# Optimization experiments

Measured on AMD Instinct MI355X. Metric: run time of the kernel, lower is better.

The kernel has to match this reference:

```python
import jax, jax.numpy as jnp
import numpy as np


def setup_inputs() -> dict:
    key = jax.random.key(0)
    k1, k2 = jax.random.split(key)
    N, C, H, W = 4, 32, 512, 512
    src = jax.random.normal(k1, (N, C, H, W), dtype=jnp.float32)
    # flow: per-pixel displacement in pixels, channels [dx, dy]
    flow = jax.random.normal(k2, (N, 2, H, W), dtype=jnp.float32) * 3.0
    return {"src": src, "flow": flow}


def reference(src, flow):
    """SpatialTransformer.forward(src, flow, train=True): identity grid + flow,
    normalize to [-1,1], then manual bilinear_grid_sample (align_corners=True)."""
    N, C, H, W = src.shape
    dt = flow.dtype

    # identity grid: stack(meshgrid(arange(H), arange(W)))[[1,0]] -> (x, y) channels
    yy, xx = jnp.meshgrid(jnp.arange(H, dtype=dt), jnp.arange(W, dtype=dt), indexing='ij')
    grid = jnp.stack([xx, yy])[None]          # (1, 2, H, W)
    new_locs = grid + flow                    # (N, 2, H, W)

    # normalize: shape = [W, H]; channel 0 (x) by W-1, channel 1 (y) by H-1
    xn = 2.0 * (new_locs[:, 0] / (W - 1) - 0.5)   # (N, H, W)
    yn = 2.0 * (new_locs[:, 1] / (H - 1) - 0.5)

    # bilinear_grid_sample, align_corners=True: unnormalize back to pixel coords
    x = (xn + 1.0) / 2.0 * (W - 1)
    y = (yn + 1.0) / 2.0 * (H - 1)

    x0 = jnp.floor(x)
    y0 = jnp.floor(y)
    x1 = x0 + 1.0
    y1 = y0 + 1.0

    wa = (x1 - x) * (y1 - y)   # weight for (x0, y0)
    wb = (x1 - x) * (y - y0)   # weight for (x0, y1)
    wc = (x - x0) * (y1 - y)   # weight for (x1, y0)
    wd = (x - x0) * (y - y0)   # weight for (x1, y1)

    # zero-pad image by 1 pixel on each side, shift indices by +1, clamp
    im_p = jnp.pad(src, ((0, 0), (0, 0), (1, 1), (1, 1)))  # (N, C, H+2, W+2)
    Hp, Wp = H + 2, W + 2
    xi0 = jnp.clip(x0.astype(jnp.int32) + 1, 0, Wp - 1)
    xi1 = jnp.clip(x1.astype(jnp.int32) + 1, 0, Wp - 1)
    yi0 = jnp.clip(y0.astype(jnp.int32) + 1, 0, Hp - 1)
    yi1 = jnp.clip(y1.astype(jnp.int32) + 1, 0, Hp - 1)

    def gather(im, yi, xi):  # im: (C, Hp, Wp); yi, xi: (H, W) -> (C, H, W)
        return im[:, yi, xi]

    Ia = jax.vmap(gather)(im_p, yi0, xi0)
    Ib = jax.vmap(gather)(im_p, yi1, xi0)
    Ic = jax.vmap(gather)(im_p, yi0, xi1)
    Id = jax.vmap(gather)(im_p, yi1, xi1)

    out = (Ia * wa[:, None] + Ib * wb[:, None]
           + Ic * wc[:, None] + Id * wd[:, None])   # (N, C, H, W)
    return out
```

## Files before the change

### kernel.cpp

```cpp
#include <hip/hip_runtime.h>
#include <hip/hip_bf16.h>


constexpr int N_ = 4, C_ = 32, H_ = 512, W_ = 512;
constexpr size_t PLANE = (size_t)H_ * W_;

__global__ __launch_bounds__(256) void nchw_to_nhwc(
    const float* __restrict__ in, float* __restrict__ out) {
    __shared__ float lds[256][33];

    int b = blockIdx.x;
    int n = b >> 10;
    int pb = (b & 1023) << 8;

    int t = threadIdx.x;

    {
        int c = t >> 3;
        int j = t & 7;
        const float* ip = in + ((size_t)n * C_ + c) * PLANE + pb;
        #pragma unroll
        for (int it = 0; it < 8; ++it) {
            int p_off = it * 32 + j * 4;
            float4 v = *(const float4*)(ip + p_off);
            lds[p_off + 0][c] = v.x;
            lds[p_off + 1][c] = v.y;
            lds[p_off + 2][c] = v.z;
            lds[p_off + 3][c] = v.w;
        }
    }
    __syncthreads();

    {
        int q = t & 7;
        int u = t >> 3;
        float* op = out + ((size_t)n * PLANE + pb) * C_;
        #pragma unroll
        for (int it = 0; it < 8; ++it) {
            int p_local = it * 32 + u;
            float4 v;
            v.x = lds[p_local][q * 4 + 0];
            v.y = lds[p_local][q * 4 + 1];
            v.z = lds[p_local][q * 4 + 2];
            v.w = lds[p_local][q * 4 + 3];
            *(float4*)(op + (size_t)p_local * C_ + q * 4) = v;
        }
    }
}

__global__ __launch_bounds__(256) void st_warp_nhwc(
    const float* __restrict__ srcT, const float* __restrict__ flow,
    float* __restrict__ out) {
    int t = blockIdx.x * blockDim.x + threadIdx.x;
    int q = t & 7;
    int g = t >> 3;

    int w = g & (W_ - 1);
    int h = (g >> 9) & (H_ - 1);
    int n = g >> 18;

    const float* f = flow + (size_t)n * 2 * PLANE + (size_t)h * W_ + w;
    float fx = f[0];
    float fy = f[PLANE];

    float xl = (float)w + fx;
    float yl = (float)h + fy;
    float xn = 2.0f * (xl / (float)(W_ - 1) - 0.5f);
    float yn = 2.0f * (yl / (float)(H_ - 1) - 0.5f);
    float x = (xn + 1.0f) / 2.0f * (float)(W_ - 1);
    float y = (yn + 1.0f) / 2.0f * (float)(H_ - 1);

    float x0f = floorf(x), y0f = floorf(y);
    float x1f = x0f + 1.0f, y1f = y0f + 1.0f;

    int ix0 = (int)x0f, iy0 = (int)y0f;

    int xa = min(max(ix0 + 1, 0), W_ + 1) - 1;
    int xb = min(max(ix0 + 2, 0), W_ + 1) - 1;
    int ya = min(max(iy0 + 1, 0), H_ + 1) - 1;
    int yb = min(max(iy0 + 2, 0), H_ + 1) - 1;

    float vxa = ((unsigned)xa < (unsigned)W_) ? 1.0f : 0.0f;
    float vxb = ((unsigned)xb < (unsigned)W_) ? 1.0f : 0.0f;
    float vya = ((unsigned)ya < (unsigned)H_) ? 1.0f : 0.0f;
    float vyb = ((unsigned)yb < (unsigned)H_) ? 1.0f : 0.0f;

    float ax = (x1f - x) * vxa;
    float bx = (x - x0f) * vxb;
    float ay = (y1f - y) * vya;
    float by = (y - y0f) * vyb;

    float wa = ax * ay;
    float wb = ax * by;
    float wc = bx * ay;
    float wd = bx * by;

    int xac = min(max(xa, 0), W_ - 1);
    int xbc = min(max(xb, 0), W_ - 1);
    int yac = min(max(ya, 0), H_ - 1);
    int ybc = min(max(yb, 0), H_ - 1);

    const float* sp = srcT + (size_t)n * PLANE * C_ + (size_t)q * 4;
    const float4 A = *(const float4*)(sp + (size_t)(yac * W_ + xac) * C_);
    const float4 B = *(const float4*)(sp + (size_t)(ybc * W_ + xac) * C_);
    const float4 Cv = *(const float4*)(sp + (size_t)(yac * W_ + xbc) * C_);
    const float4 D = *(const float4*)(sp + (size_t)(ybc * W_ + xbc) * C_);

    float r0 = A.x * wa + B.x * wb + Cv.x * wc + D.x * wd;
    float r1 = A.y * wa + B.y * wb + Cv.y * wc + D.y * wd;
    float r2 = A.z * wa + B.z * wb + Cv.z * wc + D.z * wd;
    float r3 = A.w * wa + B.w * wb + Cv.w * wc + D.w * wd;

    float* op = out + ((size_t)n * C_ + 4 * q) * PLANE + (size_t)h * W_ + w;
    op[0] = r0;
    op[PLANE] = r1;
    op[2 * PLANE] = r2;
    op[3 * PLANE] = r3;
}

__global__ __launch_bounds__(256) void st_warp_direct(
    const float* __restrict__ src, const float* __restrict__ flow,
    float* __restrict__ out) {
    int idx = blockIdx.x * blockDim.x + threadIdx.x;
    if (idx >= N_ * H_ * W_) return;
    int w = idx & (W_ - 1);
    int h = (idx >> 9) & (H_ - 1);
    int n = idx >> 18;
    const float* f = flow + (size_t)n * 2 * PLANE + (size_t)h * W_ + w;
    float fx = f[0], fy = f[PLANE];
    float xl = (float)w + fx, yl = (float)h + fy;
    float xn = 2.0f * (xl / (float)(W_ - 1) - 0.5f);
    float yn = 2.0f * (yl / (float)(H_ - 1) - 0.5f);
    float x = (xn + 1.0f) / 2.0f * (float)(W_ - 1);
    float y = (yn + 1.0f) / 2.0f * (float)(H_ - 1);
    float x0f = floorf(x), y0f = floorf(y);
    float x1f = x0f + 1.0f, y1f = y0f + 1.0f;
    int ix0 = (int)x0f, iy0 = (int)y0f;
    int xa = min(max(ix0 + 1, 0), W_ + 1) - 1;
    int xb = min(max(ix0 + 2, 0), W_ + 1) - 1;
    int ya = min(max(iy0 + 1, 0), H_ + 1) - 1;
    int yb = min(max(iy0 + 2, 0), H_ + 1) - 1;
    float vxa = ((unsigned)xa < (unsigned)W_) ? 1.0f : 0.0f;
    float vxb = ((unsigned)xb < (unsigned)W_) ? 1.0f : 0.0f;
    float vya = ((unsigned)ya < (unsigned)H_) ? 1.0f : 0.0f;
    float vyb = ((unsigned)yb < (unsigned)H_) ? 1.0f : 0.0f;
    float ax = (x1f - x) * vxa, bx = (x - x0f) * vxb;
    float ay = (y1f - y) * vya, by = (y - y0f) * vyb;
    float wa = ax * ay, wb = ax * by, wc = bx * ay, wd = bx * by;
    int xac = min(max(xa, 0), W_ - 1), xbc = min(max(xb, 0), W_ - 1);
    int yac = min(max(ya, 0), H_ - 1), ybc = min(max(yb, 0), H_ - 1);
    int o00 = yac * W_ + xac, o01 = ybc * W_ + xac;
    int o10 = yac * W_ + xbc, o11 = ybc * W_ + xbc;
    const float* sp = src + (size_t)n * C_ * PLANE;
    float* op = out + (size_t)n * C_ * PLANE + (size_t)h * W_ + w;
    #pragma unroll 4
    for (int c = 0; c < C_; ++c) {
        const float* s = sp + (size_t)c * PLANE;
        float v = s[o00] * wa + s[o01] * wb + s[o10] * wc + s[o11] * wd;
        op[(size_t)c * PLANE] = v;
    }
}

extern "C" void kernel_launch(void* const* d_in, const int* in_sizes, int n_in,
                              void* d_out, int out_size, void* d_ws, size_t ws_size,
                              hipStream_t stream) {
    const float* src  = (const float*)d_in[0];
    const float* flow = (const float*)d_in[1];
    float* out = (float*)d_out;

    const size_t need = (size_t)N_ * C_ * PLANE * sizeof(float);
    if (ws_size >= need) {
        float* srcT = (float*)d_ws;
        nchw_to_nhwc<<<4096, 256, 0, stream>>>(src, srcT);
        int total = N_ * H_ * W_ * 8;
        st_warp_nhwc<<<total / 256, 256, 0, stream>>>(srcT, flow, out);
    } else {
        int total = N_ * H_ * W_;
        st_warp_direct<<<(total + 255) / 256, 256, 0, stream>>>(src, flow, out);
    }
}
```

Measured before the change: 318.3 us.

## Process two rows per thread with swizzled block order and nontemporal stores

The warp kernel now has each thread handle two vertically adjacent output pixels for its channel quad, which halves the grid to 16384 blocks and loads flow for both rows up front. Block IDs are swizzled so that consecutively scheduled blocks land in different chunks of the image, likely to spread work across XCDs or channels while keeping gather locality. Output writes use nontemporal stores so streamed results do not pollute caches needed for the source gathers. The risks are less parallelism and more register pressure per thread, and the swizzle could hurt L2 locality if neighbouring blocks end up on different dies.

```diff
diff --git a/kernel.cpp b/kernel.cpp
--- a/kernel.cpp
+++ b/kernel.cpp
@@ -48,74 +48,89 @@
     }
 }
 
-__global__ __launch_bounds__(256) void st_warp_nhwc(
+__global__ __launch_bounds__(256) void st_warp_nhwc2(
     const float* __restrict__ srcT, const float* __restrict__ flow,
     float* __restrict__ out) {
-    int t = blockIdx.x * blockDim.x + threadIdx.x;
-    int q = t & 7;
-    int g = t >> 3;
+    int chunk = (int)gridDim.x >> 3;
+    int bid = blockIdx.x;
+    int swz = (bid & 7) * chunk + (bid >> 3);
+    int T = swz * 256 + (int)threadIdx.x;
 
-    int w = g & (W_ - 1);
-    int h = (g >> 9) & (H_ - 1);
-    int n = g >> 18;
+    int q = T & 7;
+    int s = T >> 3;
+    int w = s & (W_ - 1);
+    int h2 = (s >> 9) & (H_ / 2 - 1);
+    int n = s >> 17;
+    int h0 = h2 * 2;
 
-    const float* f = flow + (size_t)n * 2 * PLANE + (size_t)h * W_ + w;
-    float fx = f[0];
-    float fy = f[PLANE];
-
-    float xl = (float)w + fx;
-    float yl = (float)h + fy;
-    float xn = 2.0f * (xl / (float)(W_ - 1) - 0.5f);
-    float yn = 2.0f * (yl / (float)(H_ - 1) - 0.5f);
-    float x = (xn + 1.0f) / 2.0f * (float)(W_ - 1);
-    float y = (yn + 1.0f) / 2.0f * (float)(H_ - 1);
-
-    float x0f = floorf(x), y0f = floorf(y);
-    float x1f = x0f + 1.0f, y1f = y0f + 1.0f;
-
-    int ix0 = (int)x0f, iy0 = (int)y0f;
-
-    int xa = min(max(ix0 + 1, 0), W_ + 1) - 1;
-    int xb = min(max(ix0 + 2, 0), W_ + 1) - 1;
-    int ya = min(max(iy0 + 1, 0), H_ + 1) - 1;
-    int yb = min(max(iy0 + 2, 0), H_ + 1) - 1;
-
-    float vxa = ((unsigned)xa < (unsigned)W_) ? 1.0f : 0.0f;
-    float vxb = ((unsigned)xb < (unsigned)W_) ? 1.0f : 0.0f;
-    float vya = ((unsigned)ya < (unsigned)H_) ? 1.0f : 0.0f;
-    float vyb = ((unsigned)yb < (unsigned)H_) ? 1.0f : 0.0f;
-
-    float ax = (x1f - x) * vxa;
-    float bx = (x - x0f) * vxb;
-    float ay = (y1f - y) * vya;
-    float by = (y - y0f) * vyb;
-
-    float wa = ax * ay;
-    float wb = ax * by;
-    float wc = bx * ay;
-    float wd = bx * by;
-
-    int xac = min(max(xa, 0), W_ - 1);
-    int xbc = min(max(xb, 0), W_ - 1);
-    int yac = min(max(ya, 0), H_ - 1);
-    int ybc = min(max(yb, 0), H_ - 1);
+    const float* f = flow + (size_t)n * 2 * PLANE + (size_t)h0 * W_ + w;
+    float fx0 = f[0];
+    float fy0 = f[PLANE];
+    float fx1 = f[W_];
+    float fy1 = f[PLANE + W_];
 
     const float* sp = srcT + (size_t)n * PLANE * C_ + (size_t)q * 4;
-    const float4 A = *(const float4*)(sp + (size_t)(yac * W_ + xac) * C_);
-    const float4 B = *(const float4*)(sp + (size_t)(ybc * W_ + xac) * C_);
-    const float4 Cv = *(const float4*)(sp + (size_t)(yac * W_ + xbc) * C_);
-    const float4 D = *(const float4*)(sp + (size_t)(ybc * W_ + xbc) * C_);
+    float* op = out + ((size_t)n * C_ + 4 * q) * PLANE + (size_t)h0 * W_ + w;
 
-    float r0 = A.x * wa + B.x * wb + Cv.x * wc + D.x * wd;
-    float r1 = A.y * wa + B.y * wb + Cv.y * wc + D.y * wd;
-    float r2 = A.z * wa + B.z * wb + Cv.z * wc + D.z * wd;
-    float r3 = A.w * wa + B.w * wb + Cv.w * wc + D.w * wd;
+    #pragma unroll
+    for (int r = 0; r < 2; ++r) {
+        int h = h0 + r;
+        float fx = r ? fx1 : fx0;
+        float fy = r ? fy1 : fy0;
 
-    float* op = out + ((size_t)n * C_ + 4 * q) * PLANE + (size_t)h * W_ + w;
-    op[0] = r0;
-    op[PLANE] = r1;
-    op[2 * PLANE] = r2;
-    op[3 * PLANE] = r3;
+        float xl = (float)w + fx;
+        float yl = (float)h + fy;
+        float xn = 2.0f * (xl / (float)(W_ - 1) - 0.5f);
+        float yn = 2.0f * (yl / (float)(H_ - 1) - 0.5f);
+        float x = (xn + 1.0f) / 2.0f * (float)(W_ - 1);
+        float y = (yn + 1.0f) / 2.0f * (float)(H_ - 1);
+
+        float x0f = floorf(x), y0f = floorf(y);
+        float x1f = x0f + 1.0f, y1f = y0f + 1.0f;
+
+        int ix0 = (int)x0f, iy0 = (int)y0f;
+
+        int xa = min(max(ix0 + 1, 0), W_ + 1) - 1;
+        int xb = min(max(ix0 + 2, 0), W_ + 1) - 1;
+        int ya = min(max(iy0 + 1, 0), H_ + 1) - 1;
+        int yb = min(max(iy0 + 2, 0), H_ + 1) - 1;
+
+        float vxa = ((unsigned)xa < (unsigned)W_) ? 1.0f : 0.0f;
+        float vxb = ((unsigned)xb < (unsigned)W_) ? 1.0f : 0.0f;
+        float vya = ((unsigned)ya < (unsigned)H_) ? 1.0f : 0.0f;
+        float vyb = ((unsigned)yb < (unsigned)H_) ? 1.0f : 0.0f;
+
+        float ax = (x1f - x) * vxa;
+        float bx = (x - x0f) * vxb;
+        float ay = (y1f - y) * vya;
+        float by = (y - y0f) * vyb;
+
+        float wa = ax * ay;
+        float wb = ax * by;
+        float wc = bx * ay;
+        float wd = bx * by;
+
+        int xac = min(max(xa, 0), W_ - 1);
+        int xbc = min(max(xb, 0), W_ - 1);
+        int yac = min(max(ya, 0), H_ - 1);
+        int ybc = min(max(yb, 0), H_ - 1);
+
+        const float4 A  = *(const float4*)(sp + (size_t)(yac * W_ + xac) * C_);
+        const float4 B  = *(const float4*)(sp + (size_t)(ybc * W_ + xac) * C_);
+        const float4 Cv = *(const float4*)(sp + (size_t)(yac * W_ + xbc) * C_);
+        const float4 D  = *(const float4*)(sp + (size_t)(ybc * W_ + xbc) * C_);
+
+        float r0 = A.x * wa + B.x * wb + Cv.x * wc + D.x * wd;
+        float r1 = A.y * wa + B.y * wb + Cv.y * wc + D.y * wd;
+        float r2 = A.z * wa + B.z * wb + Cv.z * wc + D.z * wd;
+        float r3 = A.w * wa + B.w * wb + Cv.w * wc + D.w * wd;
+
+        float* o = op + (size_t)r * W_;
+        __builtin_nontemporal_store(r0, o);
+        __builtin_nontemporal_store(r1, o + PLANE);
+        __builtin_nontemporal_store(r2, o + 2 * PLANE);
+        __builtin_nontemporal_store(r3, o + 3 * PLANE);
+    }
 }
 
 __global__ __launch_bounds__(256) void st_warp_direct(
@@ -172,8 +187,7 @@
     if (ws_size >= need) {
         float* srcT = (float*)d_ws;
         nchw_to_nhwc<<<4096, 256, 0, stream>>>(src, srcT);
-        int total = N_ * H_ * W_ * 8;
-        st_warp_nhwc<<<total / 256, 256, 0, stream>>>(srcT, flow, out);
+        st_warp_nhwc2<<<16384, 256, 0, stream>>>(srcT, flow, out);
     } else {
         int total = N_ * H_ * W_;
         st_warp_direct<<<(total + 255) / 256, 256, 0, stream>>>(src, flow, out);
```

New measurement: 368.1 us. +15.7%, slower.
